# Kernel tuning notes

Measured on AMD Instinct MI355X. Metric: run time of the kernel, lower is better.

## Reference

```python
import jax, jax.numpy as jnp
import numpy as np

B, R, H, IN, L = 8, 128, 256, 512, 3
NH, DH = 4, H // 4  # attention heads


def _layernorm(x, g, b, eps=1e-5):
    mu = jnp.mean(x, axis=-1, keepdims=True)
    var = jnp.mean(jnp.square(x - mu), axis=-1, keepdims=True)
    return (x - mu) * jax.lax.rsqrt(var + eps) * g + b


def setup_inputs() -> dict:
    key = jax.random.key(0)
    ks = iter(jax.random.split(key, 40))
    s = 0.02
    d = {}
    d['x'] = jax.random.normal(next(ks), (B, IN), jnp.float32)
    d['We'] = jax.random.normal(next(ks), (IN, H), jnp.float32) * s
    d['be'] = jnp.zeros((H,), jnp.float32)
    # per-graph-layer params, stacked along leading L axis
    d['msg_W1'] = jax.random.normal(next(ks), (L, 2 * H, H), jnp.float32) * s
    d['msg_b1'] = jnp.zeros((L, H), jnp.float32)
    d['msg_W2'] = jax.random.normal(next(ks), (L, H, H), jnp.float32) * s
    d['msg_b2'] = jnp.zeros((L, H), jnp.float32)
    d['upd_W1'] = jax.random.normal(next(ks), (L, 2 * H, H), jnp.float32) * s
    d['upd_b1'] = jnp.zeros((L, H), jnp.float32)
    d['upd_W2'] = jax.random.normal(next(ks), (L, H, H), jnp.float32) * s
    d['upd_b2'] = jnp.zeros((L, H), jnp.float32)
    d['ln_g'] = jnp.ones((L, H), jnp.float32)
    d['ln_b'] = jnp.zeros((L, H), jnp.float32)
    d['rule_adj'] = jax.random.normal(next(ks), (R, R), jnp.float32)
    # multihead attention (4 heads)
    d['Wq'] = jax.random.normal(next(ks), (H, H), jnp.float32) * s
    d['bq'] = jnp.zeros((H,), jnp.float32)
    d['Wk'] = jax.random.normal(next(ks), (H, H), jnp.float32) * s
    d['bk'] = jnp.zeros((H,), jnp.float32)
    d['Wv'] = jax.random.normal(next(ks), (H, H), jnp.float32) * s
    d['bv'] = jnp.zeros((H,), jnp.float32)
    d['Wo'] = jax.random.normal(next(ks), (H, H), jnp.float32) * s
    d['bo'] = jnp.zeros((H,), jnp.float32)
    # readout MLP -> num_rules logits
    d['ro_W1'] = jax.random.normal(next(ks), (H, H), jnp.float32) * s
    d['ro_b1'] = jnp.zeros((H,), jnp.float32)
    d['ro_W2'] = jax.random.normal(next(ks), (H, R), jnp.float32) * s
    d['ro_b2'] = jnp.zeros((R,), jnp.float32)
    return d


def reference(x, We, be, msg_W1, msg_b1, msg_W2, msg_b2,
              upd_W1, upd_b1, upd_W2, upd_b2, ln_g, ln_b, rule_adj,
              Wq, bq, Wk, bk, Wv, bv, Wo, bo,
              ro_W1, ro_b1, ro_W2, ro_b2):
    # node encoder, broadcast to all rule-graph nodes: [B,R,H]
    h0 = x @ We + be
    h = jnp.broadcast_to(h0[:, None, :], (B, R, H))
    # rule adjacency with self-edges excluded (loop used i != j)
    A = jax.nn.sigmoid(rule_adj) * (1.0 - jnp.eye(R, dtype=rule_adj.dtype))  # [R,R]
    for l in range(L):
        # message_net(cat(h_i, h_j)) = relu(h_i@W1a + h_j@W1b + b1)@W2 + b2
        W1a, W1b = msg_W1[l][:H], msg_W1[l][H:]
        a = h @ W1a   # [B,R,H] (receiver i part)
        bb = h @ W1b  # [B,R,H] (sender j part)
        pre = jax.nn.relu(a[:, :, None, :] + bb[:, None, :, :] + msg_b1[l])  # [B,R,R,H]
        m = pre @ msg_W2[l] + msg_b2[l]  # [B,R,R,H] message from j to i
        agg = jnp.einsum('bijh,ij->bih', m, A)  # weighted sum over senders j
        # update_net(cat(h, agg))
        Wu1a, Wu1b = upd_W1[l][:H], upd_W1[l][H:]
        u = jax.nn.relu(h @ Wu1a + agg @ Wu1b + upd_b1[l]) @ upd_W2[l] + upd_b2[l]
        h = _layernorm(h + u, ln_g[l], ln_b[l])
    # multihead self-attention over nodes
    q = (h @ Wq + bq).reshape(B, R, NH, DH)
    k = (h @ Wk + bk).reshape(B, R, NH, DH)
    v = (h @ Wv + bv).reshape(B, R, NH, DH)
    logits = jnp.einsum('bqhd,bkhd->bhqk', q, k) / jnp.sqrt(jnp.float32(DH))
    attn = jax.nn.softmax(logits, axis=-1)
    pooled = jnp.einsum('bhqk,bkhd->bqhd', attn, v).reshape(B, R, H) @ Wo + bo
    g = jnp.mean(pooled, axis=1)  # [B,H]
    rule_logits = jax.nn.relu(g @ ro_W1 + ro_b1) @ ro_W2 + ro_b2
    rule_probabilities = jax.nn.softmax(rule_logits, axis=-1)  # [B,R]
    return rule_probabilities
```

## Files before the change

### kernel.cpp

```cpp
#include <hip/hip_runtime.h>
#include <math.h>

constexpr int NB  = 8;
constexpr int NR  = 128;
constexpr int HID = 256;
constexpr int NIN = 512;
constexpr int DHD = 64;
constexpr size_t SZ = (size_t)NB * NR * HID;

struct KP {
    const float *x, *We, *be, *msg_W1, *msg_b1, *msg_W2, *msg_b2;
    const float *upd_W1, *upd_b1, *upd_W2, *upd_b2, *ln_g, *ln_b, *rule_adj;
    const float *Wq, *bq, *Wk, *bk, *Wv, *bv, *Wo, *bo, *ro_W1, *ro_b1, *ro_W2, *ro_b2;
    float* out;
    float *N0, *N1, *N2;
    float *aB, *bbB, *p1B;
    float *aA, *bbA, *p1A;
    float *W2u, *mb2u, *Aw, *rsum;
    float *mW1s;
    float *h0g;
    float *c0g, *c1g;
    float *gacc;
    float *scratch;
};

__device__ __forceinline__ void gemm_core(
    float (&As)[16][68], float (&Bs)[16][64], int m0, int n0,
    const float* __restrict__ A, const float* __restrict__ B,
    float (&acc)[4][4])
{
    int tid = threadIdx.x;
    int ty = tid >> 4, tx = tid & 15;
    int arow = tid >> 2, acol = (tid & 3) << 2;
    int brow = tid >> 4, bcol = (tid & 15) << 2;
    int m = m0 + arow;

    float4 av = *(const float4*)&A[(size_t)m * HID + acol];
    float4 bv = *(const float4*)&B[(size_t)brow * HID + n0 + bcol];

    for (int k0 = 0; k0 < HID; k0 += 16) {
        As[acol + 0][arow] = av.x;
        As[acol + 1][arow] = av.y;
        As[acol + 2][arow] = av.z;
        As[acol + 3][arow] = av.w;
        *(float4*)&Bs[brow][bcol] = bv;
        __syncthreads();
        if (k0 + 16 < HID) {
            av = *(const float4*)&A[(size_t)m * HID + k0 + 16 + acol];
            bv = *(const float4*)&B[(size_t)(k0 + 16 + brow) * HID + n0 + bcol];
        }
#pragma unroll
        for (int kk = 0; kk < 16; ++kk) {
            float4 af = *(const float4*)&As[kk][ty << 2];
            float4 bf = *(const float4*)&Bs[kk][tx << 2];
            float a_[4] = {af.x, af.y, af.z, af.w};
            float b_[4] = {bf.x, bf.y, bf.z, bf.w};
#pragma unroll
            for (int i = 0; i < 4; ++i)
#pragma unroll
                for (int j = 0; j < 4; ++j) acc[i][j] += a_[i] * b_[j];
        }
        __syncthreads();
    }
}

__device__ __forceinline__ void gemv256w(
    const float* xs, const float* __restrict__ W,
    const float* __restrict__ bias, int relu, float* ys, float* red)
{
    int tid = threadIdx.x;
    int w = tid >> 6, l = tid & 63;
    float4 acc = {0.f, 0.f, 0.f, 0.f};
    const float* Wp = W + (size_t)(w * 64) * HID + l * 4;
    const float* xp = xs + w * 64;
#pragma unroll 16
    for (int kk = 0; kk < 64; ++kk) {
        float xv = xp[kk];
        float4 wv = *(const float4*)(Wp + (size_t)kk * HID);
        acc.x += xv * wv.x; acc.y += xv * wv.y;
        acc.z += xv * wv.z; acc.w += xv * wv.w;
    }
    *(float4*)&red[w * 256 + l * 4] = acc;
    __syncthreads();
    float v = red[tid] + red[256 + tid] + red[512 + tid] + red[768 + tid];
    if (bias) v += bias[tid];
    if (relu) v = fmaxf(v, 0.0f);
    ys[tid] = v;
    __syncthreads();
}

__device__ __forceinline__ void rows4_q(
    const float (&rows)[4][HID], const float* __restrict__ W,
    int col, int q, float o[4])
{
    o[0] = o[1] = o[2] = o[3] = 0.f;
    int kb = q * 64;
#pragma unroll 4
    for (int k0 = 0; k0 < 64; k0 += 4) {
        int k = kb + k0;
        float w0 = W[(size_t)(k + 0) * HID + col];
        float w1 = W[(size_t)(k + 1) * HID + col];
        float w2 = W[(size_t)(k + 2) * HID + col];
        float w3 = W[(size_t)(k + 3) * HID + col];
#pragma unroll
        for (int ii = 0; ii < 4; ++ii) {
            float4 rv = *(const float4*)&rows[ii][k];
            o[ii] += rv.x * w0 + rv.y * w1 + rv.z * w2 + rv.w * w3;
        }
    }
}

__device__ __forceinline__ void rows4_q3(
    const float (&rows)[4][HID],
    const float* __restrict__ W0, const float* __restrict__ W1,
    const float* __restrict__ W2m,
    int col, int q, float o[3][4])
{
#pragma unroll
    for (int p = 0; p < 3; ++p)
#pragma unroll
        for (int ii = 0; ii < 4; ++ii) o[p][ii] = 0.f;
    int kb = q * 64;
#pragma unroll 2
    for (int k0 = 0; k0 < 64; k0 += 4) {
        int k = kb + k0;
        float4 rv[4];
#pragma unroll
        for (int ii = 0; ii < 4; ++ii) rv[ii] = *(const float4*)&rows[ii][k];
        const float* Wp[3] = {W0, W1, W2m};
#pragma unroll
        for (int p = 0; p < 3; ++p) {
            const float* W = Wp[p];
            float w0 = W[(size_t)(k + 0) * HID + col];
            float w1 = W[(size_t)(k + 1) * HID + col];
            float w2 = W[(size_t)(k + 2) * HID + col];
            float w3 = W[(size_t)(k + 3) * HID + col];
#pragma unroll
            for (int ii = 0; ii < 4; ++ii)
                o[p][ii] += rv[ii].x * w0 + rv[ii].y * w1
                          + rv[ii].z * w2 + rv[ii].w * w3;
        }
    }
}

__global__ __launch_bounds__(256) void setup0_kernel(KP P) {
    __shared__ union {
        struct { float As[16][68]; float Bs[16][64]; } g;
        struct { float xs[NIN]; float part[8][32]; } e;
    } L;
    int blk = blockIdx.x;
    int t = threadIdx.x;

    if (blk < 32) {
        int rr = blk * 4 + (t >> 6);
        int l = t & 63;
        float s_loc = 0.f;
#pragma unroll
        for (int rep = 0; rep < 2; ++rep) {
            int j = l + rep * 64;
            float xv = P.rule_adj[rr * NR + j];
            float sg = 1.0f / (1.0f + expf(-xv));
            if (j == rr) sg = 0.0f;
            P.Aw[rr * NR + j] = sg;
            s_loc += sg;
        }
#pragma unroll
        for (int off = 32; off; off >>= 1) s_loc += __shfl_xor(s_loc, off);
        if (l == 0) P.rsum[rr] = s_loc;
    } else if (blk < 80) {
        int idx = blk - 32, l2 = idx >> 4, t16 = idx & 15;
        int m0 = (t16 >> 2) * 64, n0 = (t16 & 3) * 64;
        float acc[4][4] = {};
        gemm_core(L.g.As, L.g.Bs, m0, n0,
                  P.msg_W2 + (size_t)l2 * HID * HID,
                  P.upd_W1 + (size_t)l2 * 2 * HID * HID + (size_t)HID * HID,
                  acc);
        int ty = t >> 4, tx = t & 15;
        float* C = P.W2u + (size_t)l2 * HID * HID;
#pragma unroll
        for (int i = 0; i < 4; ++i) {
            int m = m0 + (ty << 2) + i, n = n0 + (tx << 2);
            float4 o = {acc[i][0], acc[i][1], acc[i][2], acc[i][3]};
            *(float4*)&C[(size_t)m * HID + n] = o;
        }
    } else if (blk < 83) {
        int l2 = blk - 80;
        const float* b2v = P.msg_b2 + l2 * HID;
        const float* Bm = P.upd_W1 + (size_t)l2 * 2 * HID * HID + (size_t)HID * HID;
        float acc = 0.f;
#pragma unroll 4
        for (int k = 0; k < HID; ++k) acc += b2v[k] * Bm[(size_t)k * HID + t];
        P.mb2u[l2 * HID + t] = acc;
    } else if (blk < 147) {
        int idx = blk - 83;
        int b = idx >> 3, s = idx & 7;
        L.e.xs[t]       = P.x[b * NIN + t];
        L.e.xs[256 + t] = P.x[b * NIN + 256 + t];
        __syncthreads();
        int c = t & 31, seg = t >> 5;
        int col = s * 32 + c;
        const float* Wp = P.We + (size_t)(seg * 64) * HID + col;
        const float* xp = L.e.xs + seg * 64;
        float acc = 0.f;
#pragma unroll 16
        for (int k = 0; k < 64; ++k) acc += xp[k] * Wp[(size_t)k * HID];
        L.e.part[seg][c] = acc;
        __syncthreads();
        if (t < 32) {
            float v = 0.f;
#pragma unroll
            for (int sg = 0; sg < 8; ++sg) v += L.e.part[sg][t];
            int cc = s * 32 + t;
            P.h0g[b * HID + cc] = v + P.be[cc];
        }
    } else if (blk < 163) {
        int base = (blk - 147) * 4096;
        for (int i = t; i < 4096; i += 256) {
            int o = base + i;
            P.mW1s[o] = P.msg_W1[o] + P.msg_W1[65536 + o];
        }
    } else {
        int pfid = blk - 163, npf = 256 - 163;
        const float* arr[11] = {P.We, P.msg_W1, P.msg_W2, P.upd_W1, P.upd_W2,
                                P.Wq, P.Wk, P.Wv, P.Wo, P.ro_W1, P.ro_W2};
        const int n4[11] = {32768, 98304, 49152, 98304, 49152,
                            16384, 16384, 16384, 16384, 16384, 8192};
        float s = 0.f;
        for (int a = 0; a < 11; ++a) {
            const float4* p4 = (const float4*)arr[a];
            for (int i = pfid * 256 + t; i < n4[a]; i += npf * 256) {
                float4 v = p4[i];
                s += v.x + v.y + v.z + v.w;
            }
        }
        if (s == 1.0e37f) P.scratch[pfid] = s;
    }
}

__global__ __launch_bounds__(256) void setup1_kernel(KP P) {
    __shared__ float h0s[HID], c0s[HID], p0s[HID], c1s[HID];
    __shared__ float red[1024];
    int b = blockIdx.x;
    int t = threadIdx.x;
    h0s[t] = P.h0g[b * HID + t];
    __syncthreads();
    gemv256w(h0s, P.upd_W1, nullptr, 0, c0s, red);
    gemv256w(h0s, P.mW1s, P.msg_b1, 1, p0s, red);
    gemv256w(p0s, P.W2u, P.mb2u, 0, c1s, red);
    P.c0g[b * HID + t] = c0s[t];
    P.c1g[b * HID + t] = c1s[t];
}

__global__ __launch_bounds__(1024) void layer0p_kernel(KP P) {
    __shared__ float h0s[HID];
    __shared__ float u1s[4][HID];
    __shared__ float nrm[4][HID];
    __shared__ float part3[3][4][4][HID];
    __shared__ float sred[4][4][2];
    int blk = blockIdx.x;
    int m0 = blk * 4;
    int b = m0 >> 7, i0 = m0 & 127;
    int t = threadIdx.x;
    int col = t & 255, q = t >> 8;
    int w4 = (t >> 6) & 3, l = t & 63;

    {
        float c0 = P.c0g[b * HID + col];
        float c1 = P.c1g[b * HID + col];
        if (q == 0) h0s[col] = P.h0g[b * HID + col];
        float ubv = P.upd_b1[col];
        u1s[q][col] = fmaxf(c0 + P.rsum[i0 + q] * c1 + ubv, 0.0f);
    }
    __syncthreads();

    {
        float o[4];
        rows4_q(u1s, P.upd_W2, col, q, o);
#pragma unroll
        for (int ii = 0; ii < 4; ++ii) part3[0][q][ii][col] = o[ii];
    }
    __syncthreads();

    float v;
    {
        float h0v = h0s[col] + P.upd_b2[col];
        v = part3[0][0][q][col] + part3[0][1][q][col]
          + part3[0][2][q][col] + part3[0][3][q][col] + h0v;
        float s = v, qq2 = v * v;
#pragma unroll
        for (int off = 32; off; off >>= 1) {
            s += __shfl_xor(s, off); qq2 += __shfl_xor(qq2, off);
        }
        if (l == 0) { sred[q][w4][0] = s; sred[q][w4][1] = qq2; }
    }
    __syncthreads();
    {
        float ss  = sred[q][0][0] + sred[q][1][0] + sred[q][2][0] + sred[q][3][0];
        float qq2 = sred[q][0][1] + sred[q][1][1] + sred[q][2][1] + sred[q][3][1];
        float mu = ss * (1.0f / HID);
        float inv = rsqrtf(qq2 * (1.0f / HID) - mu * mu + 1e-5f);
        float nv = (v - mu) * inv * P.ln_g[col] + P.ln_b[col];
        nrm[q][col] = nv;
        P.N0[(size_t)(m0 + q) * HID + col] = nv;
    }
    __syncthreads();

    {
        const float* mW1a1 = P.msg_W1 + (size_t)1 * 2 * HID * HID;
        const float* uW1a1 = P.upd_W1 + (size_t)1 * 2 * HID * HID;
        float o3[3][4];
        rows4_q3(nrm, mW1a1, mW1a1 + (size_t)HID * HID, uW1a1, col, q, o3);
#pragma unroll
        for (int p = 0; p < 3; ++p)
#pragma unroll
            for (int ii = 0; ii < 4; ++ii) part3[p][q][ii][col] = o3[p][ii];
    }
    __syncthreads();
    if (q < 3) {
        float* po = (q == 0) ? P.aB : (q == 1) ? P.bbB : P.p1B;
#pragma unroll
        for (int ii = 0; ii < 4; ++ii) {
            float s = part3[q][0][ii][col] + part3[q][1][ii][col]
                    + part3[q][2][ii][col] + part3[q][3][ii][col];
            po[(size_t)(m0 + ii) * HID + col] = s;
        }
    }
}

__global__ __launch_bounds__(1024) void aggproj_kernel(
    const float* __restrict__ a, const float* __restrict__ bbv,
    const float* __restrict__ mb1, const float* __restrict__ Aw,
    const float* __restrict__ rsumv,
    const float* __restrict__ P1, const float* __restrict__ W2u,
    const float* __restrict__ mb2u, const float* __restrict__ ub1,
    const float* __restrict__ uW2, const float* __restrict__ ub2,
    const float* __restrict__ Nprev, const float* __restrict__ lng,
    const float* __restrict__ lnb, float* __restrict__ Nout,
    const float* __restrict__ pw0, const float* __restrict__ pb0, float* __restrict__ o0,
    const float* __restrict__ pw1, const float* __restrict__ pb1, float* __restrict__ o1,
    const float* __restrict__ pw2, const float* __restrict__ pb2, float* __restrict__ o2,
    float* __restrict__ gzero)
{
    __shared__ float ap[4][HID];
    __shared__ float u1s[4][HID];
    __shared__ float nrm[4][HID];
    __shared__ float awr[4][NR];
    __shared__ float part3[3][4][4][HID];
    __shared__ float sred[4][4][2];
    int blk = blockIdx.x;
    int b  = blk >> 5;
    int i0 = (blk & 31) * 4;
    int m0 = b * NR + i0;
    int t  = threadIdx.x;
    int col = t & 255, q = t >> 8;
    int w4 = (t >> 6) & 3, l = t & 63;

    if (gzero && blk == 0 && q == 0) {
#pragma unroll
        for (int i = 0; i < 8; ++i) gzero[i * 256 + col] = 0.f;
    }

    if (t < 512) awr[t >> 7][t & 127] = Aw[(i0 + (t >> 7)) * NR + (t & 127)];

    float bias = mb1[col];
    float ai[4];
#pragma unroll
    for (int ii = 0; ii < 4; ++ii)
        ai[ii] = a[(size_t)(m0 + ii) * HID + col] + bias;
    __syncthreads();

    {
        float acc[4] = {0.f, 0.f, 0.f, 0.f};
        const float* bbb = &bbv[(size_t)b * NR * HID + col];
        int jb = q * 32;
#pragma unroll 4
        for (int j = 0; j < 32; ++j) {
            float bj = bbb[(size_t)(jb + j) * HID];
#pragma unroll
            for (int ii = 0; ii < 4; ++ii) {
                float pre = fmaxf(ai[ii] + bj, 0.0f);
                acc[ii] += awr[ii][jb + j] * pre;
            }
        }
#pragma unroll
        for (int ii = 0; ii < 4; ++ii) part3[0][q][ii][col] = acc[ii];
    }
    __syncthreads();
    ap[q][col] = part3[0][0][q][col] + part3[0][1][q][col]
               + part3[0][2][q][col] + part3[0][3][q][col];
    __syncthreads();

    {
        float o[4];
        rows4_q(ap, W2u, col, q, o);
#pragma unroll
        for (int ii = 0; ii < 4; ++ii) part3[0][q][ii][col] = o[ii];
    }
    __syncthreads();
    {
        float w2f = part3[0][0][q][col] + part3[0][1][q][col]
                  + part3[0][2][q][col] + part3[0][3][q][col];
        float vv = w2f + P1[(size_t)(m0 + q) * HID + col]
                 + rsumv[i0 + q] * mb2u[col] + ub1[col];
        u1s[q][col] = fmaxf(vv, 0.0f);
    }
    __syncthreads();

    {
        float o[4];
        rows4_q(u1s, uW2, col, q, o);
#pragma unroll
        for (int ii = 0; ii < 4; ++ii) part3[0][q][ii][col] = o[ii];
    }
    __syncthreads();
    float v;
    {
        float uf = part3[0][0][q][col] + part3[0][1][q][col]
                 + part3[0][2][q][col] + part3[0][3][q][col];
        v = Nprev[(size_t)(m0 + q) * HID + col] + uf + ub2[col];
        float s = v, qq2 = v * v;
#pragma unroll
        for (int off = 32; off; off >>= 1) {
            s += __shfl_xor(s, off); qq2 += __shfl_xor(qq2, off);
        }
        if (l == 0) { sred[q][w4][0] = s; sred[q][w4][1] = qq2; }
    }
    __syncthreads();
    {
        float ss  = sred[q][0][0] + sred[q][1][0] + sred[q][2][0] + sred[q][3][0];
        float qq2 = sred[q][0][1] + sred[q][1][1] + sred[q][2][1] + sred[q][3][1];
        float mu = ss * (1.0f / HID);
        float inv = rsqrtf(qq2 * (1.0f / HID) - mu * mu + 1e-5f);
        float nv = (v - mu) * inv * lng[col] + lnb[col];
        nrm[q][col] = nv;
        Nout[(size_t)(m0 + q) * HID + col] = nv;
    }
    __syncthreads();

    {
        float o3[3][4];
        rows4_q3(nrm, pw0, pw1, pw2, col, q, o3);
#pragma unroll
        for (int p = 0; p < 3; ++p)
#pragma unroll
            for (int ii = 0; ii < 4; ++ii) part3[p][q][ii][col] = o3[p][ii];
    }
    __syncthreads();
    if (q < 3) {
        const float* pb = (q == 0) ? pb0 : (q == 1) ? pb1 : pb2;
        float* po = (q == 0) ? o0 : (q == 1) ? o1 : o2;
        float pbv = pb ? pb[col] : 0.f;
#pragma unroll
        for (int ii = 0; ii < 4; ++ii) {
            float s = part3[q][0][ii][col] + part3[q][1][ii][col]
                    + part3[q][2][ii][col] + part3[q][3][ii][col] + pbv;
            po[(size_t)(m0 + ii) * HID + col] = s;
        }
    }
}

__global__ __launch_bounds__(256) void attention_kernel(
    const float* __restrict__ q, const float* __restrict__ k,
    const float* __restrict__ v, float* __restrict__ gacc)
{
    __shared__ struct { float KhT[64][128]; float S[16][128]; float qs[16][64]; } L;
    int blk = blockIdx.x;
    int bh = blk >> 3, ig = blk & 7;
    int b = bh >> 2, hd = bh & 3;
    int i0 = ig * 16;
    int t = threadIdx.x;
    const float* qg = q + ((size_t)b * NR) * HID + hd * DHD;
    const float* kg = k + ((size_t)b * NR) * HID + hd * DHD;
    const float* vg = v + ((size_t)b * NR) * HID + hd * DHD;

    {
        int j = t >> 1, half = t & 1;
        const float* krow = kg + (size_t)j * HID + half * 32;
#pragma unroll
        for (int c = 0; c < 32; c += 4) {
            float4 kv = *(const float4*)(krow + c);
            L.KhT[half * 32 + c + 0][j] = kv.x;
            L.KhT[half * 32 + c + 1][j] = kv.y;
            L.KhT[half * 32 + c + 2][j] = kv.z;
            L.KhT[half * 32 + c + 3][j] = kv.w;
        }
    }
    {
        int ii = t >> 4, d0 = (t & 15) * 4;
        *(float4*)&L.qs[ii][d0] = *(const float4*)(qg + (size_t)(i0 + ii) * HID + d0);
    }
    __syncthreads();
    {
        int j = t & 127, ii2 = t >> 7;
        float acc[8] = {0.f,0.f,0.f,0.f,0.f,0.f,0.f,0.f};
#pragma unroll 4
        for (int d = 0; d < 64; ++d) {
            float kv = L.KhT[d][j];
#pragma unroll
            for (int ii = 0; ii < 8; ++ii) acc[ii] += L.qs[ii2 * 8 + ii][d] * kv;
        }
#pragma unroll
        for (int ii = 0; ii < 8; ++ii) L.S[ii2 * 8 + ii][j] = acc[ii] * 0.125f;
    }
    __syncthreads();
    {
        int w = t >> 6, l = t & 63;
#pragma unroll
        for (int r = w * 4; r < w * 4 + 4; ++r) {
            float e0 = L.S[r][l], e1 = L.S[r][l + 64];
            float mx = fmaxf(e0, e1);
#pragma unroll
            for (int off = 32; off; off >>= 1) mx = fmaxf(mx, __shfl_xor(mx, off));
            e0 = expf(e0 - mx); e1 = expf(e1 - mx);
            float sm = e0 + e1;
#pragma unroll
            for (int off = 32; off; off >>= 1) sm += __shfl_xor(sm, off);
            float inv = 1.0f / sm;
            L.S[r][l] = e0 * inv; L.S[r][l + 64] = e1 * inv;
        }
    }
    __syncthreads();
    {
        int d = t & 63, ir = t >> 6;
        float accv[4] = {0.f, 0.f, 0.f, 0.f};
        const float* vp = vg + d;
#pragma unroll 8
        for (int j = 0; j < NR; ++j) {
            float vv = vp[(size_t)j * HID];
#pragma unroll
            for (int p = 0; p < 4; ++p) accv[p] += L.S[p * 4 + ir][j] * vv;
        }
        float s = accv[0] + accv[1] + accv[2] + accv[3];
        atomicAdd(&gacc[b * HID + hd * DHD + d], s);
    }
}

__global__ __launch_bounds__(256) void tailf_kernel(KP P) {
    __shared__ float v0[HID], v1[HID], v2[HID];
    __shared__ float red[1024];
    int b = blockIdx.x;
    int t = threadIdx.x;
    int w = t >> 6, l = t & 63;

    v0[t] = P.gacc[b * HID + t] * (1.0f / NR);
    __syncthreads();
    gemv256w(v0, P.Wo, P.bo, 0, v1, red);
    gemv256w(v1, P.ro_W1, P.ro_b1, 1, v2, red);

    {
        float2 acc = {0.f, 0.f};
        const float* Wp = P.ro_W2 + (size_t)(w * 64) * NR + l * 2;
        const float* xp = v2 + w * 64;
#pragma unroll 8
        for (int kk = 0; kk < 64; ++kk) {
            float xv = xp[kk];
            float2 wv = *(const float2*)(Wp + (size_t)kk * NR);
            acc.x += xv * wv.x; acc.y += xv * wv.y;
        }
        *(float2*)&red[w * 128 + l * 2] = acc;
        __syncthreads();
    }
    float logit = -1e30f;
    if (t < NR) logit = red[t] + red[128 + t] + red[256 + t] + red[384 + t] + P.ro_b2[t];
    __syncthreads();
    float m = logit;
#pragma unroll
    for (int off = 32; off; off >>= 1) m = fmaxf(m, __shfl_xor(m, off));
    if (l == 0) red[w] = m;
    __syncthreads();
    m = fmaxf(red[0], red[1]);
    float e = (t < NR) ? expf(logit - m) : 0.0f;
    float ssum = e;
#pragma unroll
    for (int off = 32; off; off >>= 1) ssum += __shfl_xor(ssum, off);
    if (l == 0) red[4 + w] = ssum;
    __syncthreads();
    float tot = red[4] + red[5];
    if (t < NR) P.out[b * NR + t] = e / tot;
}

extern "C" void kernel_launch(void* const* d_in, const int* in_sizes, int n_in,
                              void* d_out, int out_size, void* d_ws, size_t ws_size,
                              hipStream_t stream)
{
    KP P;
    P.x        = (const float*)d_in[0];
    P.We       = (const float*)d_in[1];
    P.be       = (const float*)d_in[2];
    P.msg_W1   = (const float*)d_in[3];
    P.msg_b1   = (const float*)d_in[4];
    P.msg_W2   = (const float*)d_in[5];
    P.msg_b2   = (const float*)d_in[6];
    P.upd_W1   = (const float*)d_in[7];
    P.upd_b1   = (const float*)d_in[8];
    P.upd_W2   = (const float*)d_in[9];
    P.upd_b2   = (const float*)d_in[10];
    P.ln_g     = (const float*)d_in[11];
    P.ln_b     = (const float*)d_in[12];
    P.rule_adj = (const float*)d_in[13];
    P.Wq       = (const float*)d_in[14];
    P.bq       = (const float*)d_in[15];
    P.Wk       = (const float*)d_in[16];
    P.bk       = (const float*)d_in[17];
    P.Wv       = (const float*)d_in[18];
    P.bv       = (const float*)d_in[19];
    P.Wo       = (const float*)d_in[20];
    P.bo       = (const float*)d_in[21];
    P.ro_W1    = (const float*)d_in[22];
    P.ro_b1    = (const float*)d_in[23];
    P.ro_W2    = (const float*)d_in[24];
    P.ro_b2    = (const float*)d_in[25];
    P.out      = (float*)d_out;

    float* b0 = (float*)d_ws;
    P.N0     = b0;  b0 += SZ;
    P.N1     = b0;  b0 += SZ;
    P.N2     = b0;  b0 += SZ;
    P.aB     = b0;  b0 += SZ;
    P.bbB    = b0;  b0 += SZ;
    P.p1B    = b0;  b0 += SZ;
    P.aA     = b0;  b0 += SZ;
    P.bbA    = b0;  b0 += SZ;
    P.p1A    = b0;  b0 += SZ;
    P.W2u    = b0;  b0 += 3 * HID * HID;
    P.mb2u   = b0;  b0 += 3 * HID;
    P.mW1s   = b0;  b0 += HID * HID;
    P.Aw     = b0;  b0 += NR * NR;
    P.rsum   = b0;  b0 += NR;
    P.h0g    = b0;  b0 += NB * HID;
    P.c0g    = b0;  b0 += NB * HID;
    P.c1g    = b0;  b0 += NB * HID;
    P.gacc   = b0;  b0 += NB * HID;
    P.scratch= b0;  b0 += 256;

    setup0_kernel<<<dim3(256), 256, 0, stream>>>(P);

    setup1_kernel<<<dim3(8), 256, 0, stream>>>(P);

    layer0p_kernel<<<dim3(256), 1024, 0, stream>>>(P);

    {
        const int l = 1;
        const float* mW1a2 = P.msg_W1 + (size_t)2 * 2 * HID * HID;
        const float* uW1a2 = P.upd_W1 + (size_t)2 * 2 * HID * HID;
        aggproj_kernel<<<dim3(256), 1024, 0, stream>>>(
            P.aB, P.bbB, P.msg_b1 + (size_t)l * HID, P.Aw, P.rsum,
            P.p1B, P.W2u + (size_t)l * HID * HID, P.mb2u + l * HID,
            P.upd_b1 + (size_t)l * HID,
            P.upd_W2 + (size_t)l * HID * HID, P.upd_b2 + (size_t)l * HID,
            P.N0, P.ln_g + (size_t)l * HID, P.ln_b + (size_t)l * HID, P.N1,
            mW1a2, nullptr, P.aA,
            mW1a2 + (size_t)HID * HID, nullptr, P.bbA,
            uW1a2, nullptr, P.p1A,
            nullptr);
    }

    {
        const int l = 2;
        aggproj_kernel<<<dim3(256), 1024, 0, stream>>>(
            P.aA, P.bbA, P.msg_b1 + (size_t)l * HID, P.Aw, P.rsum,
            P.p1A, P.W2u + (size_t)l * HID * HID, P.mb2u + l * HID,
            P.upd_b1 + (size_t)l * HID,
            P.upd_W2 + (size_t)l * HID * HID, P.upd_b2 + (size_t)l * HID,
            P.N1, P.ln_g + (size_t)l * HID, P.ln_b + (size_t)l * HID, P.N2,
            P.Wq, P.bq, P.aB,
            P.Wk, P.bk, P.bbB,
            P.Wv, P.bv, P.p1B,
            P.gacc);
    }

    attention_kernel<<<dim3(256), 256, 0, stream>>>(P.aB, P.bbB, P.p1B, P.gacc);

    tailf_kernel<<<dim3(8), 256, 0, stream>>>(P);
}
```

Baseline: 224.5 us.

## Fuse all stages into one persistent megakernel with software grid barriers

Replaces the seven separate kernel launches with a single 256-block persistent kernel. The stages are separated by atomic-counter barriers: one grid-wide barrier after setup, then per-batch barriers across 32 blocks. The aim is to remove launch gaps and inter-kernel drain time. It also switches the setup GEMM to a rows-of-4 scheme and zeroes gacc inside the kernel. This relies on all 256 blocks of 1024 threads being co-resident, which risks deadlock if they are not.

```diff
diff --git a/kernel.cpp b/kernel.cpp
--- a/kernel.cpp
+++ b/kernel.cpp
@@ -13,7 +13,7 @@
     const float *upd_W1, *upd_b1, *upd_W2, *upd_b2, *ln_g, *ln_b, *rule_adj;
     const float *Wq, *bq, *Wk, *bk, *Wv, *bv, *Wo, *bo, *ro_W1, *ro_b1, *ro_W2, *ro_b2;
     float* out;
-    float *N0, *N1, *N2;
+    float *N0, *N1;
     float *aB, *bbB, *p1B;
     float *aA, *bbA, *p1A;
     float *W2u, *mb2u, *Aw, *rsum;
@@ -22,70 +22,45 @@
     float *c0g, *c1g;
     float *gacc;
     float *scratch;
+    unsigned* bars;
 };
 
-__device__ __forceinline__ void gemm_core(
-    float (&As)[16][68], float (&Bs)[16][64], int m0, int n0,
-    const float* __restrict__ A, const float* __restrict__ B,
-    float (&acc)[4][4])
-{
-    int tid = threadIdx.x;
-    int ty = tid >> 4, tx = tid & 15;
-    int arow = tid >> 2, acol = (tid & 3) << 2;
-    int brow = tid >> 4, bcol = (tid & 15) << 2;
-    int m = m0 + arow;
-
-    float4 av = *(const float4*)&A[(size_t)m * HID + acol];
-    float4 bv = *(const float4*)&B[(size_t)brow * HID + n0 + bcol];
-
-    for (int k0 = 0; k0 < HID; k0 += 16) {
-        As[acol + 0][arow] = av.x;
-        As[acol + 1][arow] = av.y;
-        As[acol + 2][arow] = av.z;
-        As[acol + 3][arow] = av.w;
-        *(float4*)&Bs[brow][bcol] = bv;
-        __syncthreads();
-        if (k0 + 16 < HID) {
-            av = *(const float4*)&A[(size_t)m * HID + k0 + 16 + acol];
-            bv = *(const float4*)&B[(size_t)(k0 + 16 + brow) * HID + n0 + bcol];
-        }
-#pragma unroll
-        for (int kk = 0; kk < 16; ++kk) {
-            float4 af = *(const float4*)&As[kk][ty << 2];
-            float4 bf = *(const float4*)&Bs[kk][tx << 2];
-            float a_[4] = {af.x, af.y, af.z, af.w};
-            float b_[4] = {bf.x, bf.y, bf.z, bf.w};
-#pragma unroll
-            for (int i = 0; i < 4; ++i)
-#pragma unroll
-                for (int j = 0; j < 4; ++j) acc[i][j] += a_[i] * b_[j];
-        }
-        __syncthreads();
-    }
-}
-
-__device__ __forceinline__ void gemv256w(
-    const float* xs, const float* __restrict__ W,
-    const float* __restrict__ bias, int relu, float* ys, float* red)
-{
-    int tid = threadIdx.x;
-    int w = tid >> 6, l = tid & 63;
-    float4 acc = {0.f, 0.f, 0.f, 0.f};
-    const float* Wp = W + (size_t)(w * 64) * HID + l * 4;
-    const float* xp = xs + w * 64;
-#pragma unroll 16
-    for (int kk = 0; kk < 64; ++kk) {
-        float xv = xp[kk];
-        float4 wv = *(const float4*)(Wp + (size_t)kk * HID);
-        acc.x += xv * wv.x; acc.y += xv * wv.y;
-        acc.z += xv * wv.z; acc.w += xv * wv.w;
-    }
-    *(float4*)&red[w * 256 + l * 4] = acc;
-    __syncthreads();
-    float v = red[tid] + red[256 + tid] + red[512 + tid] + red[768 + tid];
-    if (bias) v += bias[tid];
-    if (relu) v = fmaxf(v, 0.0f);
-    ys[tid] = v;
+struct MainS {
+    float u1s[4][HID];
+    float nrm[4][HID];
+    float ap[4][HID];
+    float h0s[HID];
+    float awr[4][NR];
+    float sred[4][4][2];
+    float part3[3][4][4][HID];
+};
+struct AttnS {
+    float KhT[64][128];
+    float S[16][128];
+    float qs[16][64];
+    float red[16][64];
+};
+struct SetupS {
+    float rows[4][HID];
+    float part[4][4][HID];
+    float xs[NIN];
+};
+struct TailS {
+    float v0[HID], v1[HID], v2[HID];
+    float part[4][HID];
+    float led[NR], el[NR];
+};
+union ShU { MainS m; AttnS a; SetupS s; TailS tl; };
+
+__device__ __forceinline__ void sync_bar(unsigned* bar, unsigned members) {
+    __syncthreads();
+    if (threadIdx.x == 0) {
+        __threadfence();
+        unsigned ticket = atomicAdd(bar, 1u);
+        unsigned target = (ticket / members + 1u) * members;
+        while (atomicAdd(bar, 0u) < target) __builtin_amdgcn_s_sleep(8);
+        __threadfence();
+    }
     __syncthreads();
 }
 
@@ -143,17 +118,328 @@
     }
 }
 
-__global__ __launch_bounds__(256) void setup0_kernel(KP P) {
-    __shared__ union {
-        struct { float As[16][68]; float Bs[16][64]; } g;
-        struct { float xs[NIN]; float part[8][32]; } e;
-    } L;
-    int blk = blockIdx.x;
-    int t = threadIdx.x;
-
-    if (blk < 32) {
-        int rr = blk * 4 + (t >> 6);
-        int l = t & 63;
+__device__ __forceinline__ float gemv_q(
+    const float* xs, const float* __restrict__ W, int col, int q)
+{
+    float o = 0.f;
+    int kb = q * 64;
+#pragma unroll 8
+    for (int k = 0; k < 64; ++k)
+        o += xs[kb + k] * W[(size_t)(kb + k) * HID + col];
+    return o;
+}
+
+__device__ void aggproj_stage(ShU& sh, const KP& P, int b, int i0, int m0, int t,
+    const float* __restrict__ a, const float* __restrict__ bbv,
+    const float* __restrict__ mb1,
+    const float* __restrict__ P1, const float* __restrict__ W2u,
+    const float* __restrict__ mb2u, const float* __restrict__ ub1,
+    const float* __restrict__ uW2, const float* __restrict__ ub2,
+    const float* __restrict__ Nprev, const float* __restrict__ lng,
+    const float* __restrict__ lnb, float* __restrict__ Nout,
+    const float* __restrict__ pw0, const float* __restrict__ pb0, float* __restrict__ o0,
+    const float* __restrict__ pw1, const float* __restrict__ pb1, float* __restrict__ o1,
+    const float* __restrict__ pw2, const float* __restrict__ pb2, float* __restrict__ o2)
+{
+    int col = t & 255, q = t >> 8;
+    int w4 = (t >> 6) & 3, l = t & 63;
+
+    if (t < 512) sh.m.awr[t >> 7][t & 127] = P.Aw[(i0 + (t >> 7)) * NR + (t & 127)];
+
+    float bias = mb1[col];
+    float ai[4];
+#pragma unroll
+    for (int ii = 0; ii < 4; ++ii)
+        ai[ii] = a[(size_t)(m0 + ii) * HID + col] + bias;
+    __syncthreads();
+
+    {
+        float acc[4] = {0.f, 0.f, 0.f, 0.f};
+        const float* bbb = &bbv[(size_t)b * NR * HID + col];
+        int jb = q * 32;
+#pragma unroll 4
+        for (int j = 0; j < 32; ++j) {
+            float bj = bbb[(size_t)(jb + j) * HID];
+#pragma unroll
+            for (int ii = 0; ii < 4; ++ii) {
+                float pre = fmaxf(ai[ii] + bj, 0.0f);
+                acc[ii] += sh.m.awr[ii][jb + j] * pre;
+            }
+        }
+#pragma unroll
+        for (int ii = 0; ii < 4; ++ii) sh.m.part3[0][q][ii][col] = acc[ii];
+    }
+    __syncthreads();
+    sh.m.ap[q][col] = sh.m.part3[0][0][q][col] + sh.m.part3[0][1][q][col]
+                    + sh.m.part3[0][2][q][col] + sh.m.part3[0][3][q][col];
+    __syncthreads();
+
+    {
+        float o[4];
+        rows4_q(sh.m.ap, W2u, col, q, o);
+#pragma unroll
+        for (int ii = 0; ii < 4; ++ii) sh.m.part3[0][q][ii][col] = o[ii];
+    }
+    __syncthreads();
+    {
+        float w2f = sh.m.part3[0][0][q][col] + sh.m.part3[0][1][q][col]
+                  + sh.m.part3[0][2][q][col] + sh.m.part3[0][3][q][col];
+        float vv = w2f + P1[(size_t)(m0 + q) * HID + col]
+                 + P.rsum[i0 + q] * mb2u[col] + ub1[col];
+        sh.m.u1s[q][col] = fmaxf(vv, 0.0f);
+    }
+    __syncthreads();
+
+    {
+        float o[4];
+        rows4_q(sh.m.u1s, uW2, col, q, o);
+#pragma unroll
+        for (int ii = 0; ii < 4; ++ii) sh.m.part3[0][q][ii][col] = o[ii];
+    }
+    __syncthreads();
+    float v;
+    {
+        float uf = sh.m.part3[0][0][q][col] + sh.m.part3[0][1][q][col]
+                 + sh.m.part3[0][2][q][col] + sh.m.part3[0][3][q][col];
+        v = Nprev[(size_t)(m0 + q) * HID + col] + uf + ub2[col];
+        float s = v, qq2 = v * v;
+#pragma unroll
+        for (int off = 32; off; off >>= 1) {
+            s += __shfl_xor(s, off); qq2 += __shfl_xor(qq2, off);
+        }
+        if (l == 0) { sh.m.sred[q][w4][0] = s; sh.m.sred[q][w4][1] = qq2; }
+    }
+    __syncthreads();
+    {
+        float ss  = sh.m.sred[q][0][0] + sh.m.sred[q][1][0]
+                  + sh.m.sred[q][2][0] + sh.m.sred[q][3][0];
+        float qq2 = sh.m.sred[q][0][1] + sh.m.sred[q][1][1]
+                  + sh.m.sred[q][2][1] + sh.m.sred[q][3][1];
+        float mu = ss * (1.0f / HID);
+        float inv = rsqrtf(qq2 * (1.0f / HID) - mu * mu + 1e-5f);
+        float nv = (v - mu) * inv * lng[col] + lnb[col];
+        sh.m.nrm[q][col] = nv;
+        if (Nout) Nout[(size_t)(m0 + q) * HID + col] = nv;
+    }
+    __syncthreads();
+
+    {
+        float o3[3][4];
+        rows4_q3(sh.m.nrm, pw0, pw1, pw2, col, q, o3);
+#pragma unroll
+        for (int p = 0; p < 3; ++p)
+#pragma unroll
+            for (int ii = 0; ii < 4; ++ii) sh.m.part3[p][q][ii][col] = o3[p][ii];
+    }
+    __syncthreads();
+    if (q < 3) {
+        const float* pb = (q == 0) ? pb0 : (q == 1) ? pb1 : pb2;
+        float* po = (q == 0) ? o0 : (q == 1) ? o1 : o2;
+        float pbv = pb ? pb[col] : 0.f;
+#pragma unroll
+        for (int ii = 0; ii < 4; ++ii) {
+            float s = sh.m.part3[q][0][ii][col] + sh.m.part3[q][1][ii][col]
+                    + sh.m.part3[q][2][ii][col] + sh.m.part3[q][3][ii][col] + pbv;
+            po[(size_t)(m0 + ii) * HID + col] = s;
+        }
+    }
+}
+
+__device__ void layer0_stage(ShU& sh, const KP& P, int b, int i0, int m0, int t)
+{
+    int col = t & 255, q = t >> 8;
+    int w4 = (t >> 6) & 3, l = t & 63;
+
+    {
+        float c0 = P.c0g[b * HID + col];
+        float c1 = P.c1g[b * HID + col];
+        if (q == 0) sh.m.h0s[col] = P.h0g[b * HID + col];
+        sh.m.u1s[q][col] = fmaxf(c0 + P.rsum[i0 + q] * c1 + P.upd_b1[col], 0.0f);
+    }
+    __syncthreads();
+
+    {
+        float o[4];
+        rows4_q(sh.m.u1s, P.upd_W2, col, q, o);
+#pragma unroll
+        for (int ii = 0; ii < 4; ++ii) sh.m.part3[0][q][ii][col] = o[ii];
+    }
+    __syncthreads();
+
+    float v;
+    {
+        float h0v = sh.m.h0s[col] + P.upd_b2[col];
+        v = sh.m.part3[0][0][q][col] + sh.m.part3[0][1][q][col]
+          + sh.m.part3[0][2][q][col] + sh.m.part3[0][3][q][col] + h0v;
+        float s = v, qq2 = v * v;
+#pragma unroll
+        for (int off = 32; off; off >>= 1) {
+            s += __shfl_xor(s, off); qq2 += __shfl_xor(qq2, off);
+        }
+        if (l == 0) { sh.m.sred[q][w4][0] = s; sh.m.sred[q][w4][1] = qq2; }
+    }
+    __syncthreads();
+    {
+        float ss  = sh.m.sred[q][0][0] + sh.m.sred[q][1][0]
+                  + sh.m.sred[q][2][0] + sh.m.sred[q][3][0];
+        float qq2 = sh.m.sred[q][0][1] + sh.m.sred[q][1][1]
+                  + sh.m.sred[q][2][1] + sh.m.sred[q][3][1];
+        float mu = ss * (1.0f / HID);
+        float inv = rsqrtf(qq2 * (1.0f / HID) - mu * mu + 1e-5f);
+        float nv = (v - mu) * inv * P.ln_g[col] + P.ln_b[col];
+        sh.m.nrm[q][col] = nv;
+        P.N0[(size_t)(m0 + q) * HID + col] = nv;
+    }
+    __syncthreads();
+
+    {
+        const float* mW1a1 = P.msg_W1 + (size_t)1 * 2 * HID * HID;
+        const float* uW1a1 = P.upd_W1 + (size_t)1 * 2 * HID * HID;
+        float o3[3][4];
+        rows4_q3(sh.m.nrm, mW1a1, mW1a1 + (size_t)HID * HID, uW1a1, col, q, o3);
+#pragma unroll
+        for (int p = 0; p < 3; ++p)
+#pragma unroll
+            for (int ii = 0; ii < 4; ++ii) sh.m.part3[p][q][ii][col] = o3[p][ii];
+    }
+    __syncthreads();
+    if (q < 3) {
+        float* po = (q == 0) ? P.aB : (q == 1) ? P.bbB : P.p1B;
+#pragma unroll
+        for (int ii = 0; ii < 4; ++ii) {
+            float s = sh.m.part3[q][0][ii][col] + sh.m.part3[q][1][ii][col]
+                    + sh.m.part3[q][2][ii][col] + sh.m.part3[q][3][ii][col];
+            po[(size_t)(m0 + ii) * HID + col] = s;
+        }
+    }
+}
+
+__device__ void attn_stage(AttnS& A, const KP& P, int b, int sl, int t)
+{
+    int hd = sl >> 3, ig = sl & 7, i0q = ig * 16;
+    const float* qg = P.aB  + ((size_t)b * NR) * HID + hd * DHD;
+    const float* kg = P.bbB + ((size_t)b * NR) * HID + hd * DHD;
+    const float* vg = P.p1B + ((size_t)b * NR) * HID + hd * DHD;
+
+    {
+        int j = t >> 3, seg = t & 7;
+        const float* kr = kg + (size_t)j * HID + seg * 8;
+        float4 a4 = *(const float4*)kr;
+        float4 b4 = *(const float4*)(kr + 4);
+        A.KhT[seg * 8 + 0][j] = a4.x; A.KhT[seg * 8 + 1][j] = a4.y;
+        A.KhT[seg * 8 + 2][j] = a4.z; A.KhT[seg * 8 + 3][j] = a4.w;
+        A.KhT[seg * 8 + 4][j] = b4.x; A.KhT[seg * 8 + 5][j] = b4.y;
+        A.KhT[seg * 8 + 6][j] = b4.z; A.KhT[seg * 8 + 7][j] = b4.w;
+    }
+    {
+        int ii = t >> 6, d = t & 63;
+        A.qs[ii][d] = qg[(size_t)(i0q + ii) * HID + d];
+    }
+    __syncthreads();
+    {
+        int j = t & 127, ii2 = t >> 7;
+        float a0 = 0.f, a1 = 0.f;
+#pragma unroll 4
+        for (int d = 0; d < 64; ++d) {
+            float kv = A.KhT[d][j];
+            a0 += A.qs[2 * ii2][d] * kv;
+            a1 += A.qs[2 * ii2 + 1][d] * kv;
+        }
+        A.S[2 * ii2][j] = a0 * 0.125f;
+        A.S[2 * ii2 + 1][j] = a1 * 0.125f;
+    }
+    __syncthreads();
+    {
+        int w = t >> 6, l = t & 63;
+        float e0 = A.S[w][l], e1 = A.S[w][l + 64];
+        float mx = fmaxf(e0, e1);
+#pragma unroll
+        for (int off = 32; off; off >>= 1) mx = fmaxf(mx, __shfl_xor(mx, off));
+        e0 = expf(e0 - mx); e1 = expf(e1 - mx);
+        float sm = e0 + e1;
+#pragma unroll
+        for (int off = 32; off; off >>= 1) sm += __shfl_xor(sm, off);
+        float inv = 1.0f / sm;
+        A.S[w][l] = e0 * inv; A.S[w][l + 64] = e1 * inv;
+    }
+    __syncthreads();
+    {
+        int r = t >> 6, d = t & 63;
+        float acc = 0.f;
+        const float* vp = vg + d;
+#pragma unroll 8
+        for (int j = 0; j < NR; ++j) acc += A.S[r][j] * vp[(size_t)j * HID];
+        A.red[r][d] = acc;
+    }
+    __syncthreads();
+    if (t < 64) {
+        float s = 0.f;
+#pragma unroll
+        for (int r = 0; r < 16; ++r) s += A.red[r][t];
+        atomicAdd(&P.gacc[b * HID + hd * DHD + t], s);
+    }
+}
+
+__device__ void tail_stage(TailS& T, const KP& P, int b, int t)
+{
+    int col = t & 255, q = t >> 8;
+    if (t < 256) T.v0[t] = P.gacc[b * HID + t] * (1.0f / NR);
+    __syncthreads();
+    T.part[q][col] = gemv_q(T.v0, P.Wo, col, q);
+    __syncthreads();
+    if (q == 0)
+        T.v1[col] = T.part[0][col] + T.part[1][col] + T.part[2][col]
+                  + T.part[3][col] + P.bo[col];
+    __syncthreads();
+    T.part[q][col] = gemv_q(T.v1, P.ro_W1, col, q);
+    __syncthreads();
+    if (q == 0)
+        T.v2[col] = fmaxf(T.part[0][col] + T.part[1][col] + T.part[2][col]
+                        + T.part[3][col] + P.ro_b1[col], 0.0f);
+    __syncthreads();
+    {
+        int j = t & 127, q8 = t >> 7;
+        int kb = q8 * 32;
+        float acc = 0.f;
+#pragma unroll 8
+        for (int k2 = 0; k2 < 32; ++k2)
+            acc += T.v2[kb + k2] * P.ro_W2[(size_t)(kb + k2) * NR + j];
+        float* pp = &T.part[0][0];
+        pp[q8 * 128 + j] = acc;
+    }
+    __syncthreads();
+    if (t < NR) {
+        float* pp = &T.part[0][0];
+        float s = 0.f;
+#pragma unroll
+        for (int p8 = 0; p8 < 8; ++p8) s += pp[p8 * 128 + t];
+        T.led[t] = s + P.ro_b2[t];
+    }
+    __syncthreads();
+    if (t < NR) {
+        float m = -1e30f;
+        for (int j = 0; j < NR; ++j) m = fmaxf(m, T.led[j]);
+        T.el[t] = expf(T.led[t] - m);
+    }
+    __syncthreads();
+    if (t < NR) {
+        float tot = 0.f;
+        for (int j = 0; j < NR; ++j) tot += T.el[j];
+        P.out[b * NR + t] = T.el[t] / tot;
+    }
+}
+
+__global__ __launch_bounds__(1024) void mega_kernel(KP P)
+{
+    __shared__ ShU sh;
+    int blk = blockIdx.x, t = threadIdx.x;
+    int b = blk >> 5, sl = blk & 31;
+    int i0 = sl * 4, m0 = b * NR + i0;
+    unsigned* gbar = P.bars;
+    unsigned* bbar = P.bars + 16 + b * 16;
+
+    if (blk < 8) {
+        int rr = blk * 16 + (t >> 6), l = t & 63;
         float s_loc = 0.f;
 #pragma unroll
         for (int rep = 0; rep < 2; ++rep) {
@@ -167,416 +453,147 @@
 #pragma unroll
         for (int off = 32; off; off >>= 1) s_loc += __shfl_xor(s_loc, off);
         if (l == 0) P.rsum[rr] = s_loc;
-    } else if (blk < 80) {
-        int idx = blk - 32, l2 = idx >> 4, t16 = idx & 15;
-        int m0 = (t16 >> 2) * 64, n0 = (t16 & 3) * 64;
-        float acc[4][4] = {};
-        gemm_core(L.g.As, L.g.Bs, m0, n0,
-                  P.msg_W2 + (size_t)l2 * HID * HID,
-                  P.upd_W1 + (size_t)l2 * 2 * HID * HID + (size_t)HID * HID,
-                  acc);
-        int ty = t >> 4, tx = t & 15;
+        if (blk == 0) { P.gacc[t] = 0.f; P.gacc[1024 + t] = 0.f; }
+    } else if (blk < 56) {
+        int idx = blk - 8, l2 = idx / 16, rb = idx % 16;
+        const float* A = P.msg_W2 + (size_t)l2 * HID * HID;
+        const float* B = P.upd_W1 + (size_t)l2 * 2 * HID * HID + (size_t)HID * HID;
         float* C = P.W2u + (size_t)l2 * HID * HID;
-#pragma unroll
-        for (int i = 0; i < 4; ++i) {
-            int m = m0 + (ty << 2) + i, n = n0 + (tx << 2);
-            float4 o = {acc[i][0], acc[i][1], acc[i][2], acc[i][3]};
-            *(float4*)&C[(size_t)m * HID + n] = o;
-        }
-    } else if (blk < 83) {
-        int l2 = blk - 80;
-        const float* b2v = P.msg_b2 + l2 * HID;
-        const float* Bm = P.upd_W1 + (size_t)l2 * 2 * HID * HID + (size_t)HID * HID;
+        int col = t & 255, q = t >> 8;
+        for (int rd = 0; rd < 4; ++rd) {
+            int row0 = rb * 16 + rd * 4;
+            sh.s.rows[q][col] = A[(size_t)(row0 + q) * HID + col];
+            __syncthreads();
+            float o[4];
+            rows4_q(sh.s.rows, B, col, q, o);
+#pragma unroll
+            for (int ii = 0; ii < 4; ++ii) sh.s.part[q][ii][col] = o[ii];
+            __syncthreads();
+            C[(size_t)(row0 + q) * HID + col] =
+                sh.s.part[0][q][col] + sh.s.part[1][q][col]
+              + sh.s.part[2][q][col] + sh.s.part[3][q][col];
+            __syncthreads();
+        }
+    } else if (blk < 59) {
+        int l2 = blk - 56;
+        if (t < 256) {
+            const float* b2v = P.msg_b2 + l2 * HID;
+            const float* Bm = P.upd_W1 + (size_t)l2 * 2 * HID * HID + (size_t)HID * HID;
+            float acc = 0.f;
+#pragma unroll 4
+            for (int k = 0; k < HID; ++k) acc += b2v[k] * Bm[(size_t)k * HID + t];
+            P.mb2u[l2 * HID + t] = acc;
+        }
+    } else if (blk < 67) {
+        int bb = blk - 59;
+        if (t < NIN) sh.s.xs[t] = P.x[bb * NIN + t];
+        __syncthreads();
+        int col = t & 255, q = t >> 8;
         float acc = 0.f;
-#pragma unroll 4
-        for (int k = 0; k < HID; ++k) acc += b2v[k] * Bm[(size_t)k * HID + t];
-        P.mb2u[l2 * HID + t] = acc;
-    } else if (blk < 147) {
-        int idx = blk - 83;
-        int b = idx >> 3, s = idx & 7;
-        L.e.xs[t]       = P.x[b * NIN + t];
-        L.e.xs[256 + t] = P.x[b * NIN + 256 + t];
+        int kb = q * 128;
+#pragma unroll 8
+        for (int k = 0; k < 128; ++k)
+            acc += sh.s.xs[kb + k] * P.We[(size_t)(kb + k) * HID + col];
+        sh.s.part[q][0][col] = acc;
         __syncthreads();
-        int c = t & 31, seg = t >> 5;
-        int col = s * 32 + c;
-        const float* Wp = P.We + (size_t)(seg * 64) * HID + col;
-        const float* xp = L.e.xs + seg * 64;
-        float acc = 0.f;
-#pragma unroll 16
-        for (int k = 0; k < 64; ++k) acc += xp[k] * Wp[(size_t)k * HID];
-        L.e.part[seg][c] = acc;
-        __syncthreads();
-        if (t < 32) {
-            float v = 0.f;
-#pragma unroll
-            for (int sg = 0; sg < 8; ++sg) v += L.e.part[sg][t];
-            int cc = s * 32 + t;
-            P.h0g[b * HID + cc] = v + P.be[cc];
-        }
-    } else if (blk < 163) {
-        int base = (blk - 147) * 4096;
-        for (int i = t; i < 4096; i += 256) {
+        if (q == 0)
+            P.h0g[bb * HID + col] = sh.s.part[0][0][col] + sh.s.part[1][0][col]
+                                  + sh.s.part[2][0][col] + sh.s.part[3][0][col]
+                                  + P.be[col];
+    } else if (blk < 71) {
+        int idx4 = blk - 67;
+        int base = idx4 * 16384;
+        for (int i = t; i < 16384; i += 1024) {
             int o = base + i;
             P.mW1s[o] = P.msg_W1[o] + P.msg_W1[65536 + o];
         }
     } else {
-        int pfid = blk - 163, npf = 256 - 163;
+        int pfid = blk - 71, npf = 185;
         const float* arr[11] = {P.We, P.msg_W1, P.msg_W2, P.upd_W1, P.upd_W2,
                                 P.Wq, P.Wk, P.Wv, P.Wo, P.ro_W1, P.ro_W2};
         const int n4[11] = {32768, 98304, 49152, 98304, 49152,
                             16384, 16384, 16384, 16384, 16384, 8192};
         float s = 0.f;
-        for (int a = 0; a < 11; ++a) {
-            const float4* p4 = (const float4*)arr[a];
-            for (int i = pfid * 256 + t; i < n4[a]; i += npf * 256) {
+        for (int a2 = 0; a2 < 11; ++a2) {
+            const float4* p4 = (const float4*)arr[a2];
+            for (int i = pfid * 1024 + t; i < n4[a2]; i += npf * 1024) {
                 float4 v = p4[i];
                 s += v.x + v.y + v.z + v.w;
             }
         }
         if (s == 1.0e37f) P.scratch[pfid] = s;
     }
-}
-
-__global__ __launch_bounds__(256) void setup1_kernel(KP P) {
-    __shared__ float h0s[HID], c0s[HID], p0s[HID], c1s[HID];
-    __shared__ float red[1024];
-    int b = blockIdx.x;
-    int t = threadIdx.x;
-    h0s[t] = P.h0g[b * HID + t];
-    __syncthreads();
-    gemv256w(h0s, P.upd_W1, nullptr, 0, c0s, red);
-    gemv256w(h0s, P.mW1s, P.msg_b1, 1, p0s, red);
-    gemv256w(p0s, P.W2u, P.mb2u, 0, c1s, red);
-    P.c0g[b * HID + t] = c0s[t];
-    P.c1g[b * HID + t] = c1s[t];
-}
-
-__global__ __launch_bounds__(1024) void layer0p_kernel(KP P) {
-    __shared__ float h0s[HID];
-    __shared__ float u1s[4][HID];
-    __shared__ float nrm[4][HID];
-    __shared__ float part3[3][4][4][HID];
-    __shared__ float sred[4][4][2];
-    int blk = blockIdx.x;
-    int m0 = blk * 4;
-    int b = m0 >> 7, i0 = m0 & 127;
-    int t = threadIdx.x;
-    int col = t & 255, q = t >> 8;
-    int w4 = (t >> 6) & 3, l = t & 63;
-
-    {
-        float c0 = P.c0g[b * HID + col];
-        float c1 = P.c1g[b * HID + col];
-        if (q == 0) h0s[col] = P.h0g[b * HID + col];
-        float ubv = P.upd_b1[col];
-        u1s[q][col] = fmaxf(c0 + P.rsum[i0 + q] * c1 + ubv, 0.0f);
-    }
-    __syncthreads();
-
-    {
-        float o[4];
-        rows4_q(u1s, P.upd_W2, col, q, o);
-#pragma unroll
-        for (int ii = 0; ii < 4; ++ii) part3[0][q][ii][col] = o[ii];
-    }
-    __syncthreads();
-
-    float v;
-    {
-        float h0v = h0s[col] + P.upd_b2[col];
-        v = part3[0][0][q][col] + part3[0][1][q][col]
-          + part3[0][2][q][col] + part3[0][3][q][col] + h0v;
-        float s = v, qq2 = v * v;
-#pragma unroll
-        for (int off = 32; off; off >>= 1) {
-            s += __shfl_xor(s, off); qq2 += __shfl_xor(qq2, off);
-        }
-        if (l == 0) { sred[q][w4][0] = s; sred[q][w4][1] = qq2; }
-    }
-    __syncthreads();
-    {
-        float ss  = sred[q][0][0] + sred[q][1][0] + sred[q][2][0] + sred[q][3][0];
-        float qq2 = sred[q][0][1] + sred[q][1][1] + sred[q][2][1] + sred[q][3][1];
-        float mu = ss * (1.0f / HID);
-        float inv = rsqrtf(qq2 * (1.0f / HID) - mu * mu + 1e-5f);
-        float nv = (v - mu) * inv * P.ln_g[col] + P.ln_b[col];
-        nrm[q][col] = nv;
-        P.N0[(size_t)(m0 + q) * HID + col] = nv;
-    }
-    __syncthreads();
-
-    {
-        const float* mW1a1 = P.msg_W1 + (size_t)1 * 2 * HID * HID;
-        const float* uW1a1 = P.upd_W1 + (size_t)1 * 2 * HID * HID;
-        float o3[3][4];
-        rows4_q3(nrm, mW1a1, mW1a1 + (size_t)HID * HID, uW1a1, col, q, o3);
-#pragma unroll
-        for (int p = 0; p < 3; ++p)
-#pragma unroll
-            for (int ii = 0; ii < 4; ++ii) part3[p][q][ii][col] = o3[p][ii];
-    }
-    __syncthreads();
-    if (q < 3) {
-        float* po = (q == 0) ? P.aB : (q == 1) ? P.bbB : P.p1B;
-#pragma unroll
-        for (int ii = 0; ii < 4; ++ii) {
-            float s = part3[q][0][ii][col] + part3[q][1][ii][col]
-                    + part3[q][2][ii][col] + part3[q][3][ii][col];
-            po[(size_t)(m0 + ii) * HID + col] = s;
-        }
-    }
-}
-
-__global__ __launch_bounds__(1024) void aggproj_kernel(
-    const float* __restrict__ a, const float* __restrict__ bbv,
-    const float* __restrict__ mb1, const float* __restrict__ Aw,
-    const float* __restrict__ rsumv,
-    const float* __restrict__ P1, const float* __restrict__ W2u,
-    const float* __restrict__ mb2u, const float* __restrict__ ub1,
-    const float* __restrict__ uW2, const float* __restrict__ ub2,
-    const float* __restrict__ Nprev, const float* __restrict__ lng,
-    const float* __restrict__ lnb, float* __restrict__ Nout,
-    const float* __restrict__ pw0, const float* __restrict__ pb0, float* __restrict__ o0,
-    const float* __restrict__ pw1, const float* __restrict__ pb1, float* __restrict__ o1,
-    const float* __restrict__ pw2, const float* __restrict__ pb2, float* __restrict__ o2,
-    float* __restrict__ gzero)
-{
-    __shared__ float ap[4][HID];
-    __shared__ float u1s[4][HID];
-    __shared__ float nrm[4][HID];
-    __shared__ float awr[4][NR];
-    __shared__ float part3[3][4][4][HID];
-    __shared__ float sred[4][4][2];
-    int blk = blockIdx.x;
-    int b  = blk >> 5;
-    int i0 = (blk & 31) * 4;
-    int m0 = b * NR + i0;
-    int t  = threadIdx.x;
-    int col = t & 255, q = t >> 8;
-    int w4 = (t >> 6) & 3, l = t & 63;
-
-    if (gzero && blk == 0 && q == 0) {
-#pragma unroll
-        for (int i = 0; i < 8; ++i) gzero[i * 256 + col] = 0.f;
-    }
-
-    if (t < 512) awr[t >> 7][t & 127] = Aw[(i0 + (t >> 7)) * NR + (t & 127)];
-
-    float bias = mb1[col];
-    float ai[4];
-#pragma unroll
-    for (int ii = 0; ii < 4; ++ii)
-        ai[ii] = a[(size_t)(m0 + ii) * HID + col] + bias;
-    __syncthreads();
-
-    {
-        float acc[4] = {0.f, 0.f, 0.f, 0.f};
-        const float* bbb = &bbv[(size_t)b * NR * HID + col];
-        int jb = q * 32;
-#pragma unroll 4
-        for (int j = 0; j < 32; ++j) {
-            float bj = bbb[(size_t)(jb + j) * HID];
-#pragma unroll
-            for (int ii = 0; ii < 4; ++ii) {
-                float pre = fmaxf(ai[ii] + bj, 0.0f);
-                acc[ii] += awr[ii][jb + j] * pre;
-            }
-        }
-#pragma unroll
-        for (int ii = 0; ii < 4; ++ii) part3[0][q][ii][col] = acc[ii];
-    }
-    __syncthreads();
-    ap[q][col] = part3[0][0][q][col] + part3[0][1][q][col]
-               + part3[0][2][q][col] + part3[0][3][q][col];
-    __syncthreads();
-
-    {
-        float o[4];
-        rows4_q(ap, W2u, col, q, o);
-#pragma unroll
-        for (int ii = 0; ii < 4; ++ii) part3[0][q][ii][col] = o[ii];
-    }
-    __syncthreads();
-    {
-        float w2f = part3[0][0][q][col] + part3[0][1][q][col]
-                  + part3[0][2][q][col] + part3[0][3][q][col];
-        float vv = w2f + P1[(size_t)(m0 + q) * HID + col]
-                 + rsumv[i0 + q] * mb2u[col] + ub1[col];
-        u1s[q][col] = fmaxf(vv, 0.0f);
-    }
-    __syncthreads();
-
-    {
-        float o[4];
-        rows4_q(u1s, uW2, col, q, o);
-#pragma unroll
-        for (int ii = 0; ii < 4; ++ii) part3[0][q][ii][col] = o[ii];
-    }
-    __syncthreads();
-    float v;
-    {
-        float uf = part3[0][0][q][col] + part3[0][1][q][col]
-                 + part3[0][2][q][col] + part3[0][3][q][col];
-        v = Nprev[(size_t)(m0 + q) * HID + col] + uf + ub2[col];
-        float s = v, qq2 = v * v;
-#pragma unroll
-        for (int off = 32; off; off >>= 1) {
-            s += __shfl_xor(s, off); qq2 += __shfl_xor(qq2, off);
-        }
-        if (l == 0) { sred[q][w4][0] = s; sred[q][w4][1] = qq2; }
-    }
-    __syncthreads();
-    {
-        float ss  = sred[q][0][0] + sred[q][1][0] + sred[q][2][0] + sred[q][3][0];
-        float qq2 = sred[q][0][1] + sred[q][1][1] + sred[q][2][1] + sred[q][3][1];
-        float mu = ss * (1.0f / HID);
-        float inv = rsqrtf(qq2 * (1.0f / HID) - mu * mu + 1e-5f);
-        float nv = (v - mu) * inv * lng[col] + lnb[col];
-        nrm[q][col] = nv;
-        Nout[(size_t)(m0 + q) * HID + col] = nv;
-    }
-    __syncthreads();
-
-    {
-        float o3[3][4];
-        rows4_q3(nrm, pw0, pw1, pw2, col, q, o3);
-#pragma unroll
-        for (int p = 0; p < 3; ++p)
-#pragma unroll
-            for (int ii = 0; ii < 4; ++ii) part3[p][q][ii][col] = o3[p][ii];
-    }
-    __syncthreads();
-    if (q < 3) {
-        const float* pb = (q == 0) ? pb0 : (q == 1) ? pb1 : pb2;
-        float* po = (q == 0) ? o0 : (q == 1) ? o1 : o2;
-        float pbv = pb ? pb[col] : 0.f;
-#pragma unroll
-        for (int ii = 0; ii < 4; ++ii) {
-            float s = part3[q][0][ii][col] + part3[q][1][ii][col]
-                    + part3[q][2][ii][col] + part3[q][3][ii][col] + pbv;
-            po[(size_t)(m0 + ii) * HID + col] = s;
-        }
-    }
-}
-
-__global__ __launch_bounds__(256) void attention_kernel(
-    const float* __restrict__ q, const float* __restrict__ k,
-    const float* __restrict__ v, float* __restrict__ gacc)
-{
-    __shared__ struct { float KhT[64][128]; float S[16][128]; float qs[16][64]; } L;
-    int blk = blockIdx.x;
-    int bh = blk >> 3, ig = blk & 7;
-    int b = bh >> 2, hd = bh & 3;
-    int i0 = ig * 16;
-    int t = threadIdx.x;
-    const float* qg = q + ((size_t)b * NR) * HID + hd * DHD;
-    const float* kg = k + ((size_t)b * NR) * HID + hd * DHD;
-    const float* vg = v + ((size_t)b * NR) * HID + hd * DHD;
-
-    {
-        int j = t >> 1, half = t & 1;
-        const float* krow = kg + (size_t)j * HID + half * 32;
-#pragma unroll
-        for (int c = 0; c < 32; c += 4) {
-            float4 kv = *(const float4*)(krow + c);
-            L.KhT[half * 32 + c + 0][j] = kv.x;
-            L.KhT[half * 32 + c + 1][j] = kv.y;
-            L.KhT[half * 32 + c + 2][j] = kv.z;
-            L.KhT[half * 32 + c + 3][j] = kv.w;
-        }
-    }
-    {
-        int ii = t >> 4, d0 = (t & 15) * 4;
-        *(float4*)&L.qs[ii][d0] = *(const float4*)(qg + (size_t)(i0 + ii) * HID + d0);
-    }
-    __syncthreads();
-    {
-        int j = t & 127, ii2 = t >> 7;
-        float acc[8] = {0.f,0.f,0.f,0.f,0.f,0.f,0.f,0.f};
-#pragma unroll 4
-        for (int d = 0; d < 64; ++d) {
-            float kv = L.KhT[d][j];
-#pragma unroll
-            for (int ii = 0; ii < 8; ++ii) acc[ii] += L.qs[ii2 * 8 + ii][d] * kv;
-        }
-#pragma unroll
-        for (int ii = 0; ii < 8; ++ii) L.S[ii2 * 8 + ii][j] = acc[ii] * 0.125f;
-    }
-    __syncthreads();
-    {
-        int w = t >> 6, l = t & 63;
-#pragma unroll
-        for (int r = w * 4; r < w * 4 + 4; ++r) {
-            float e0 = L.S[r][l], e1 = L.S[r][l + 64];
-            float mx = fmaxf(e0, e1);
-#pragma unroll
-            for (int off = 32; off; off >>= 1) mx = fmaxf(mx, __shfl_xor(mx, off));
-            e0 = expf(e0 - mx); e1 = expf(e1 - mx);
-            float sm = e0 + e1;
-#pragma unroll
-            for (int off = 32; off; off >>= 1) sm += __shfl_xor(sm, off);
-            float inv = 1.0f / sm;
-            L.S[r][l] = e0 * inv; L.S[r][l + 64] = e1 * inv;
-        }
-    }
-    __syncthreads();
-    {
-        int d = t & 63, ir = t >> 6;
-        float accv[4] = {0.f, 0.f, 0.f, 0.f};
-        const float* vp = vg + d;
-#pragma unroll 8
-        for (int j = 0; j < NR; ++j) {
-            float vv = vp[(size_t)j * HID];
-#pragma unroll
-            for (int p = 0; p < 4; ++p) accv[p] += L.S[p * 4 + ir][j] * vv;
-        }
-        float s = accv[0] + accv[1] + accv[2] + accv[3];
-        atomicAdd(&gacc[b * HID + hd * DHD + d], s);
-    }
-}
-
-__global__ __launch_bounds__(256) void tailf_kernel(KP P) {
-    __shared__ float v0[HID], v1[HID], v2[HID];
-    __shared__ float red[1024];
-    int b = blockIdx.x;
-    int t = threadIdx.x;
-    int w = t >> 6, l = t & 63;
-
-    v0[t] = P.gacc[b * HID + t] * (1.0f / NR);
-    __syncthreads();
-    gemv256w(v0, P.Wo, P.bo, 0, v1, red);
-    gemv256w(v1, P.ro_W1, P.ro_b1, 1, v2, red);
-
-    {
-        float2 acc = {0.f, 0.f};
-        const float* Wp = P.ro_W2 + (size_t)(w * 64) * NR + l * 2;
-        const float* xp = v2 + w * 64;
-#pragma unroll 8
-        for (int kk = 0; kk < 64; ++kk) {
-            float xv = xp[kk];
-            float2 wv = *(const float2*)(Wp + (size_t)kk * NR);
-            acc.x += xv * wv.x; acc.y += xv * wv.y;
-        }
-        *(float2*)&red[w * 128 + l * 2] = acc;
+    sync_bar(gbar, 256);
+
+    if (sl == 0) {
+        int col = t & 255, q = t >> 8;
+        if (t < 256) sh.m.h0s[t] = P.h0g[b * HID + t];
         __syncthreads();
-    }
-    float logit = -1e30f;
-    if (t < NR) logit = red[t] + red[128 + t] + red[256 + t] + red[384 + t] + P.ro_b2[t];
-    __syncthreads();
-    float m = logit;
-#pragma unroll
-    for (int off = 32; off; off >>= 1) m = fmaxf(m, __shfl_xor(m, off));
-    if (l == 0) red[w] = m;
-    __syncthreads();
-    m = fmaxf(red[0], red[1]);
-    float e = (t < NR) ? expf(logit - m) : 0.0f;
-    float ssum = e;
-#pragma unroll
-    for (int off = 32; off; off >>= 1) ssum += __shfl_xor(ssum, off);
-    if (l == 0) red[4 + w] = ssum;
-    __syncthreads();
-    float tot = red[4] + red[5];
-    if (t < NR) P.out[b * NR + t] = e / tot;
+        float o0 = gemv_q(sh.m.h0s, P.upd_W1, col, q);
+        float o1 = gemv_q(sh.m.h0s, P.mW1s, col, q);
+        sh.m.part3[0][q][0][col] = o0;
+        sh.m.part3[0][q][1][col] = o1;
+        __syncthreads();
+        if (q == 0) {
+            float c0 = sh.m.part3[0][0][0][col] + sh.m.part3[0][1][0][col]
+                     + sh.m.part3[0][2][0][col] + sh.m.part3[0][3][0][col];
+            float pv = sh.m.part3[0][0][1][col] + sh.m.part3[0][1][1][col]
+                     + sh.m.part3[0][2][1][col] + sh.m.part3[0][3][1][col]
+                     + P.msg_b1[col];
+            sh.m.u1s[0][col] = c0;
+            sh.m.u1s[1][col] = fmaxf(pv, 0.0f);
+        }
+        __syncthreads();
+        float o2 = gemv_q(sh.m.u1s[1], P.W2u, col, q);
+        sh.m.part3[0][q][0][col] = o2;
+        __syncthreads();
+        if (q == 0) {
+            float c1 = sh.m.part3[0][0][0][col] + sh.m.part3[0][1][0][col]
+                     + sh.m.part3[0][2][0][col] + sh.m.part3[0][3][0][col]
+                     + P.mb2u[col];
+            P.c0g[b * HID + col] = sh.m.u1s[0][col];
+            P.c1g[b * HID + col] = c1;
+        }
+    }
+    sync_bar(bbar, 32);
+
+    layer0_stage(sh, P, b, i0, m0, t);
+    sync_bar(bbar, 32);
+
+    {
+        const int l = 1;
+        const float* mW1a2 = P.msg_W1 + (size_t)2 * 2 * HID * HID;
+        const float* uW1a2 = P.upd_W1 + (size_t)2 * 2 * HID * HID;
+        aggproj_stage(sh, P, b, i0, m0, t,
+            P.aB, P.bbB, P.msg_b1 + (size_t)l * HID,
+            P.p1B, P.W2u + (size_t)l * HID * HID, P.mb2u + l * HID,
+            P.upd_b1 + (size_t)l * HID,
+            P.upd_W2 + (size_t)l * HID * HID, P.upd_b2 + (size_t)l * HID,
+            P.N0, P.ln_g + (size_t)l * HID, P.ln_b + (size_t)l * HID, P.N1,
+            mW1a2, nullptr, P.aA,
+            mW1a2 + (size_t)HID * HID, nullptr, P.bbA,
+            uW1a2, nullptr, P.p1A);
+    }
+    sync_bar(bbar, 32);
+
+    {
+        const int l = 2;
+        aggproj_stage(sh, P, b, i0, m0, t,
+            P.aA, P.bbA, P.msg_b1 + (size_t)l * HID,
+            P.p1A, P.W2u + (size_t)l * HID * HID, P.mb2u + l * HID,
+            P.upd_b1 + (size_t)l * HID,
+            P.upd_W2 + (size_t)l * HID * HID, P.upd_b2 + (size_t)l * HID,
+            P.N1, P.ln_g + (size_t)l * HID, P.ln_b + (size_t)l * HID, nullptr,
+            P.Wq, P.bq, P.aB,
+            P.Wk, P.bk, P.bbB,
+            P.Wv, P.bv, P.p1B);
+    }
+    sync_bar(bbar, 32);
+
+    attn_stage(sh.a, P, b, sl, t);
+    sync_bar(bbar, 32);
+
+    if (sl == 0) tail_stage(sh.tl, P, b, t);
 }
 
 extern "C" void kernel_launch(void* const* d_in, const int* in_sizes, int n_in,
@@ -615,7 +632,6 @@
     float* b0 = (float*)d_ws;
     P.N0     = b0;  b0 += SZ;
     P.N1     = b0;  b0 += SZ;
-    P.N2     = b0;  b0 += SZ;
     P.aB     = b0;  b0 += SZ;
     P.bbB    = b0;  b0 += SZ;
     P.p1B    = b0;  b0 += SZ;
@@ -632,44 +648,9 @@
     P.c1g    = b0;  b0 += NB * HID;
     P.gacc   = b0;  b0 += NB * HID;
     P.scratch= b0;  b0 += 256;
-
-    setup0_kernel<<<dim3(256), 256, 0, stream>>>(P);
-
-    setup1_kernel<<<dim3(8), 256, 0, stream>>>(P);
-
-    layer0p_kernel<<<dim3(256), 1024, 0, stream>>>(P);
-
-    {
-        const int l = 1;
-        const float* mW1a2 = P.msg_W1 + (size_t)2 * 2 * HID * HID;
-        const float* uW1a2 = P.upd_W1 + (size_t)2 * 2 * HID * HID;
-        aggproj_kernel<<<dim3(256), 1024, 0, stream>>>(
-            P.aB, P.bbB, P.msg_b1 + (size_t)l * HID, P.Aw, P.rsum,
-            P.p1B, P.W2u + (size_t)l * HID * HID, P.mb2u + l * HID,
-            P.upd_b1 + (size_t)l * HID,
-            P.upd_W2 + (size_t)l * HID * HID, P.upd_b2 + (size_t)l * HID,
-            P.N0, P.ln_g + (size_t)l * HID, P.ln_b + (size_t)l * HID, P.N1,
-            mW1a2, nullptr, P.aA,
-            mW1a2 + (size_t)HID * HID, nullptr, P.bbA,
-            uW1a2, nullptr, P.p1A,
-            nullptr);
-    }
-
-    {
-        const int l = 2;
-        aggproj_kernel<<<dim3(256), 1024, 0, stream>>>(
-            P.aA, P.bbA, P.msg_b1 + (size_t)l * HID, P.Aw, P.rsum,
-            P.p1A, P.W2u + (size_t)l * HID * HID, P.mb2u + l * HID,
-            P.upd_b1 + (size_t)l * HID,
-            P.upd_W2 + (size_t)l * HID * HID, P.upd_b2 + (size_t)l * HID,
-            P.N1, P.ln_g + (size_t)l * HID, P.ln_b + (size_t)l * HID, P.N2,
-            P.Wq, P.bq, P.aB,
-            P.Wk, P.bk, P.bbB,
-            P.Wv, P.bv, P.p1B,
-            P.gacc);
-    }
-
-    attention_kernel<<<dim3(256), 256, 0, stream>>>(P.aB, P.bbB, P.p1B, P.gacc);
-
-    tailf_kernel<<<dim3(8), 256, 0, stream>>>(P);
-}
+    P.bars   = (unsigned*)b0; b0 += 256;
+
+    hipMemsetAsync((void*)P.bars, 0, 256 * sizeof(unsigned), stream);
+
+    mega_kernel<<<dim3(256), 1024, 0, stream>>>(P);
+}
```

New measurement: 289.6 us. +29.0%, slower.
